# Kernel optimization log

Hardware: AMD Instinct MI355X
Metric: run time of the kernel (lower is better)

## Reference

```python
import jax, jax.numpy as jnp
import numpy as np

D_MODEL = 1024
NUM_HEADS = 16
D_K = D_MODEL // NUM_HEADS


def setup_inputs() -> dict:
    key = jax.random.key(0)
    ks = jax.random.split(key, 9)
    s = 1.0 / np.sqrt(D_MODEL)
    x = jax.random.normal(ks[0], (4, 2048, D_MODEL), dtype=jnp.float32)
    Wq = jax.random.uniform(ks[1], (D_MODEL, D_MODEL), jnp.float32, -s, s)
    bq = jax.random.uniform(ks[2], (D_MODEL,), jnp.float32, -s, s)
    Wk = jax.random.uniform(ks[3], (D_MODEL, D_MODEL), jnp.float32, -s, s)
    bk = jax.random.uniform(ks[4], (D_MODEL,), jnp.float32, -s, s)
    Wv = jax.random.uniform(ks[5], (D_MODEL, D_MODEL), jnp.float32, -s, s)
    bv = jax.random.uniform(ks[6], (D_MODEL,), jnp.float32, -s, s)
    Wo = jax.random.uniform(ks[7], (D_MODEL, D_MODEL), jnp.float32, -s, s)
    bo = jax.random.uniform(ks[8], (D_MODEL,), jnp.float32, -s, s)
    return {"x": x, "Wq": Wq, "bq": bq, "Wk": Wk, "bk": bk,
            "Wv": Wv, "bv": bv, "Wo": Wo, "bo": bo}


def reference(x, Wq, bq, Wk, bk, Wv, bv, Wo, bo):
    B, S, _ = x.shape
    # Linear projections (torch Linear: x @ W.T + b)
    q = x @ Wq.T + bq
    k = x @ Wk.T + bk
    v = x @ Wv.T + bv
    # [B, H, S, d_k]
    q = q.reshape(B, S, NUM_HEADS, D_K).transpose(0, 2, 1, 3)
    k = k.reshape(B, S, NUM_HEADS, D_K).transpose(0, 2, 1, 3)
    v = v.reshape(B, S, NUM_HEADS, D_K).transpose(0, 2, 1, 3)
    score = jnp.einsum('bhqd,bhkd->bhqk', q, k) / jnp.sqrt(jnp.float32(D_K))
    causal = jnp.tril(jnp.ones((S, S), dtype=bool))  # True = keep
    score = jnp.where(causal[None, None], score, -jnp.inf)
    attn = jax.nn.softmax(score, axis=-1)
    out = jnp.einsum('bhqk,bhkd->bhqd', attn, v)
    out = out.transpose(0, 2, 1, 3).reshape(B, S, D_MODEL)
    return out @ Wo.T + bo
```

## Files before the change

### kernel.cpp

```cpp
#include <hip/hip_runtime.h>
#include <hip/hip_bf16.h>
#include <stdint.h>

#define D_MODEL 1024
#define SEQ     2048
#define BATCH   4
#define NHEAD   16
#define DKH     64
#define MTOT    (BATCH * SEQ)

typedef __bf16 bf16x8 __attribute__((ext_vector_type(8)));
typedef __bf16 bf16x4 __attribute__((ext_vector_type(4)));
typedef float  floatx4 __attribute__((ext_vector_type(4)));
typedef short  s16x4  __attribute__((ext_vector_type(4)));

#define GLOAD_LDS16(gp, lp)                                            \
    __builtin_amdgcn_global_load_lds(                                  \
        (const __attribute__((address_space(1))) unsigned int*)(gp),   \
        (__attribute__((address_space(3))) unsigned int*)(lp), 16, 0, 0)

#define MFMA16(a, b, c) __builtin_amdgcn_mfma_f32_16x16x32_bf16(a, b, c, 0, 0, 0)

#if __has_builtin(__builtin_amdgcn_exp2f)
#define EXP2(x) __builtin_amdgcn_exp2f(x)
#else
#define EXP2(x) exp2f(x)
#endif

static __device__ __forceinline__ floatx4 pv_mfma(s16x4 a, s16x4 b, floatx4 c)
{
#if __has_builtin(__builtin_amdgcn_mfma_f32_16x16x16bf16_1k)
    return __builtin_amdgcn_mfma_f32_16x16x16bf16_1k(a, b, c, 0, 0, 0);
#else
    asm("v_mfma_f32_16x16x16_bf16 %0, %1, %2, %0" : "+v"(c) : "v"(a), "v"(b));
    return c;
#endif
}

__global__ __launch_bounds__(256)
void cvt_x_kernel(const float* __restrict__ src, __bf16* __restrict__ dst)
{
    const int i = (blockIdx.x * 256 + threadIdx.x) * 4;
    floatx4 v = *(const floatx4*)(src + i);
    bf16x4 o;
    o[0] = (__bf16)v[0]; o[1] = (__bf16)v[1]; o[2] = (__bf16)v[2]; o[3] = (__bf16)v[3];
    *(bf16x4*)(dst + i) = o;
}

__global__ __launch_bounds__(256)
void cvt_w3_kernel(const float* __restrict__ Wq, const float* __restrict__ Wk,
                   const float* __restrict__ Wv, __bf16* __restrict__ Wcat)
{
    const int z = blockIdx.y;
    const float* src = (z == 0) ? Wq : ((z == 1) ? Wk : Wv);
    const int i = (blockIdx.x * 256 + threadIdx.x) * 4;
    floatx4 v = *(const floatx4*)(src + i);
    bf16x4 o;
    o[0] = (__bf16)v[0]; o[1] = (__bf16)v[1]; o[2] = (__bf16)v[2]; o[3] = (__bf16)v[3];
    *(bf16x4*)(Wcat + (size_t)z * (D_MODEL * D_MODEL) + i) = o;
}

__global__ __launch_bounds__(256)
void qkv_gemm_kernel(const __bf16* __restrict__ xb, const __bf16* __restrict__ Wcat,
                     const float* __restrict__ bq, const float* __restrict__ bk,
                     const float* __restrict__ bv,
                     __bf16* __restrict__ Q, __bf16* __restrict__ K,
                     __bf16* __restrict__ Vt)
{
    __shared__ __align__(16) char smem_raw[128 * 136 * 2];
    __bf16* As = (__bf16*)smem_raw;
    __bf16* Bs = (__bf16*)(smem_raw + 8192);
    __bf16* Cs = (__bf16*)smem_raw;

    const int t    = threadIdx.x;
    const int w    = t >> 6, l = t & 63, quad = l >> 4, r16 = l & 15;
    const int wm   = w & 1, wn = w >> 1;
    const int m0   = blockIdx.y * 128;
    const int n0   = blockIdx.x * 128;
    const int z    = n0 >> 10;
    const float* bias = (z == 0) ? bq : ((z == 1) ? bk : bv);
    __bf16* outQK     = (z == 0) ? Q  : K;
    const float scale = (z == 0) ? 0.18033688011112042f : 1.0f;

    floatx4 acc[4][4];
#pragma unroll
    for (int i = 0; i < 4; ++i)
#pragma unroll
        for (int j = 0; j < 4; ++j) acc[i][j] = (floatx4){0.f, 0.f, 0.f, 0.f};

    const int c0 = t, c1 = t + 256;
    const __bf16* Ag0 = xb   + (size_t)(m0 + (c0 >> 2)) * 1024 + (c0 & 3) * 8;
    const __bf16* Ag1 = xb   + (size_t)(m0 + (c1 >> 2)) * 1024 + (c1 & 3) * 8;
    const __bf16* Bg0 = Wcat + (size_t)(n0 + (c0 >> 2)) * 1024 + (c0 & 3) * 8;
    const __bf16* Bg1 = Wcat + (size_t)(n0 + (c1 >> 2)) * 1024 + (c1 & 3) * 8;
    unsigned int* lAs = (unsigned int*)As;
    unsigned int* lBs = (unsigned int*)Bs;

    for (int k0 = 0; k0 < 1024; k0 += 32) {
        __syncthreads();
        GLOAD_LDS16(Ag0 + k0, lAs + c0 * 4);
        GLOAD_LDS16(Ag1 + k0, lAs + c1 * 4);
        GLOAD_LDS16(Bg0 + k0, lBs + c0 * 4);
        GLOAD_LDS16(Bg1 + k0, lBs + c1 * 4);
        __syncthreads();

        bf16x8 af[4], bfm[4];
#pragma unroll
        for (int i = 0; i < 4; ++i)
            af[i] = *(const bf16x8*)&As[(wm * 64 + i * 16 + r16) * 32 + quad * 8];
#pragma unroll
        for (int j = 0; j < 4; ++j)
            bfm[j] = *(const bf16x8*)&Bs[(wn * 64 + j * 16 + r16) * 32 + quad * 8];
#pragma unroll
        for (int i = 0; i < 4; ++i)
#pragma unroll
            for (int j = 0; j < 4; ++j)
                acc[i][j] = MFMA16(af[i], bfm[j], acc[i][j]);
    }

    __syncthreads();

    if (z == 2) {
#pragma unroll
        for (int i = 0; i < 4; ++i) {
            const int mb = wm * 64 + i * 16 + quad * 4;
#pragma unroll
            for (int j = 0; j < 4; ++j) {
                const int nl = wn * 64 + j * 16 + r16;
                const float bb = bias[(n0 + nl) & 1023];
                bf16x4 p4;
#pragma unroll
                for (int r = 0; r < 4; ++r) p4[r] = (__bf16)(acc[i][j][r] + bb);
                *(bf16x4*)&Cs[nl * 136 + mb] = p4;
            }
        }
    } else {
#pragma unroll
        for (int i = 0; i < 4; ++i) {
            const int mb = wm * 64 + i * 16 + quad * 4;
#pragma unroll
            for (int j = 0; j < 4; ++j) {
                const int nl = wn * 64 + j * 16 + r16;
                const float bb = bias[(n0 + nl) & 1023];
#pragma unroll
                for (int r = 0; r < 4; ++r)
                    Cs[(mb + r) * 136 + nl] =
                        (__bf16)((acc[i][j][r] + bb) * scale);
            }
        }
    }
    __syncthreads();

    const int b  = m0 >> 11;
    if (z == 2) {
#pragma unroll
        for (int k = 0; k < 8; ++k) {
            const int nl = (t >> 4) + k * 16;
            const int ml = (t & 15) * 8;
            bf16x8 row = *(const bf16x8*)&Cs[nl * 136 + ml];
            const int f = (n0 + nl) & 1023, h = f >> 6, d = f & 63;
            const int s = (m0 & 2047) + ml;
            *(bf16x8*)&Vt[((size_t)((b * 16 + h) * 64 + d) << 11) + s] = row;
        }
    } else {
#pragma unroll
        for (int k = 0; k < 8; ++k) {
            const int ml = (t >> 4) + k * 16;
            const int nl = (t & 15) * 8;
            bf16x8 row = *(const bf16x8*)&Cs[ml * 136 + nl];
            const int f = (n0 + nl) & 1023, h = f >> 6, d = f & 63;
            const int s = (m0 & 2047) + ml;
            *(bf16x8*)&outQK[((size_t)(b * 16 + h) << 17) + ((size_t)s << 6) + d]
                = row;
        }
    }
}

__global__ __launch_bounds__(256)
void out_gemm_kernel(const __bf16* __restrict__ A, const __bf16* __restrict__ Wob,
                     const float* __restrict__ bo, float* __restrict__ out)
{
    __shared__ __align__(16) __bf16 As[128 * 32];
    __shared__ __align__(16) __bf16 Bs[128 * 32];

    const int t    = threadIdx.x;
    const int w    = t >> 6, l = t & 63, quad = l >> 4, r16 = l & 15;
    const int wm   = w & 1, wn = w >> 1;
    const int m0   = blockIdx.y * 128;
    const int n0   = blockIdx.x * 128;

    floatx4 acc[4][4];
#pragma unroll
    for (int i = 0; i < 4; ++i)
#pragma unroll
        for (int j = 0; j < 4; ++j) acc[i][j] = (floatx4){0.f, 0.f, 0.f, 0.f};

    const int c0 = t, c1 = t + 256;
    const __bf16* Ag0 = A   + (size_t)(m0 + (c0 >> 2)) * 1024 + (c0 & 3) * 8;
    const __bf16* Ag1 = A   + (size_t)(m0 + (c1 >> 2)) * 1024 + (c1 & 3) * 8;
    const __bf16* Bg0 = Wob + (size_t)(n0 + (c0 >> 2)) * 1024 + (c0 & 3) * 8;
    const __bf16* Bg1 = Wob + (size_t)(n0 + (c1 >> 2)) * 1024 + (c1 & 3) * 8;
    unsigned int* lAs = (unsigned int*)As;
    unsigned int* lBs = (unsigned int*)Bs;

    for (int k0 = 0; k0 < 1024; k0 += 32) {
        __syncthreads();
        GLOAD_LDS16(Ag0 + k0, lAs + c0 * 4);
        GLOAD_LDS16(Ag1 + k0, lAs + c1 * 4);
        GLOAD_LDS16(Bg0 + k0, lBs + c0 * 4);
        GLOAD_LDS16(Bg1 + k0, lBs + c1 * 4);
        __syncthreads();

        bf16x8 af[4], bfm[4];
#pragma unroll
        for (int i = 0; i < 4; ++i)
            af[i] = *(const bf16x8*)&As[(wm * 64 + i * 16 + r16) * 32 + quad * 8];
#pragma unroll
        for (int j = 0; j < 4; ++j)
            bfm[j] = *(const bf16x8*)&Bs[(wn * 64 + j * 16 + r16) * 32 + quad * 8];
#pragma unroll
        for (int i = 0; i < 4; ++i)
#pragma unroll
            for (int j = 0; j < 4; ++j)
                acc[i][j] = MFMA16(af[i], bfm[j], acc[i][j]);
    }

#pragma unroll
    for (int i = 0; i < 4; ++i) {
        const int mg = m0 + wm * 64 + i * 16 + quad * 4;
#pragma unroll
        for (int j = 0; j < 4; ++j) {
            const int ng = n0 + wn * 64 + j * 16 + r16;
            const float bb = bo[ng];
#pragma unroll
            for (int r = 0; r < 4; ++r)
                out[(size_t)(mg + r) * 1024 + ng] = acc[i][j][r] + bb;
        }
    }
}

__global__ __launch_bounds__(256, 4)
void attn_kernel(const __bf16* __restrict__ Qg, const __bf16* __restrict__ Kg,
                 const __bf16* __restrict__ Vtg, __bf16* __restrict__ O)
{
    __shared__ __align__(16) __bf16 Ks[2][64 * 72];
    __shared__ __align__(16) __bf16 Vs[2][64 * 72];

    const int t    = threadIdx.x;
    const int w    = t >> 6, l = t & 63, quad = l >> 4, r16 = l & 15;
    const int bh   = blockIdx.x;
    const int y    = blockIdx.y;
    const int p    = y >> 1, half = y & 1;
    const int qa   = 15 - p, qb = p;
    const size_t base = (size_t)bh * SEQ * DKH;
    const int d0   = 2 * qa + half;
    const int d1   = 2 * qb + half;
    const int nkt  = d0 + 1;
    const int row0 = qa * 128 + half * 64 + w * 16;
    const int row1 = qb * 128 + half * 64 + w * 16;

    const s16x4 ones16 = {(short)0x3F80, (short)0x3F80,
                          (short)0x3F80, (short)0x3F80};

    bf16x8 qf00, qf01, qf10, qf11;
    qf00 = *(const bf16x8*)&Qg[base + (size_t)(row0 + r16) * 64 + quad * 8];
    qf01 = *(const bf16x8*)&Qg[base + (size_t)(row0 + r16) * 64 + 32 + quad * 8];
    qf10 = *(const bf16x8*)&Qg[base + (size_t)(row1 + r16) * 64 + quad * 8];
    qf11 = *(const bf16x8*)&Qg[base + (size_t)(row1 + r16) * 64 + 32 + quad * 8];

    floatx4 o[2][4];
#pragma unroll
    for (int mi = 0; mi < 2; ++mi)
#pragma unroll
        for (int j = 0; j < 4; ++j) o[mi][j] = (floatx4){0.f, 0.f, 0.f, 0.f};
    floatx4 osum[2];
    osum[0] = (floatx4){0.f, 0.f, 0.f, 0.f};
    osum[1] = (floatx4){0.f, 0.f, 0.f, 0.f};

    const int srow = t >> 3;
    const int sg   = (t & 7) * 8;

    bf16x8 kc0, kc1, vc0, vc1;
    kc0 = *(const bf16x8*)&Kg[base + (size_t)srow * 64 + sg];
    kc1 = *(const bf16x8*)&Kg[base + (size_t)(32 + srow) * 64 + sg];
    vc0 = *(const bf16x8*)&Vtg[base + (size_t)srow * 2048 + sg];
    vc1 = *(const bf16x8*)&Vtg[base + (size_t)(32 + srow) * 2048 + sg];

    for (int kt = 0; kt < nkt; ++kt) {
        __bf16* ks = Ks[kt & 1];
        __bf16* vs = Vs[kt & 1];
        *(bf16x8*)&ks[srow * 72 + sg] = kc0;
        *(bf16x8*)&ks[(32 + srow) * 72 + sg] = kc1;
        *(bf16x8*)&vs[srow * 72 + sg] = vc0;
        *(bf16x8*)&vs[(32 + srow) * 72 + sg] = vc1;
        if (kt + 1 < nkt) {
            const int kr = (kt + 1) * 64;
            kc0 = *(const bf16x8*)&Kg[base + (size_t)(kr + srow) * 64 + sg];
            kc1 = *(const bf16x8*)&Kg[base + (size_t)(kr + 32 + srow) * 64 + sg];
            vc0 = *(const bf16x8*)&Vtg[base + (size_t)srow * 2048 + kr + sg];
            vc1 = *(const bf16x8*)&Vtg[base + (size_t)(32 + srow) * 2048 + kr + sg];
        }
        __syncthreads();

        const bool a1 = (kt <= d1);
        __builtin_amdgcn_s_setprio(1);
        bf16x8 kf0, kf1;
#pragma unroll
        for (int j = 0; j < 4; ++j) {
            kf0 = *(const bf16x8*)&ks[(j * 16 + r16) * 72 + quad * 8];
            kf1 = *(const bf16x8*)&ks[(j * 16 + r16) * 72 + 32 + quad * 8];
            floatx4 z0 = (floatx4){0.f, 0.f, 0.f, 0.f};
            floatx4 z1 = (floatx4){0.f, 0.f, 0.f, 0.f};
            z0 = MFMA16(kf0, qf00, z0);
            z0 = MFMA16(kf1, qf01, z0);
            if (a1) {
                z1 = MFMA16(kf0, qf10, z1);
                z1 = MFMA16(kf1, qf11, z1);
            }
            const int kg = kt * 64 + j * 16 + quad * 4;
            bf16x4 pb0, pb1;
            if (kt < d0) {
#pragma unroll
                for (int r = 0; r < 4; ++r)
                    pb0[r] = (__bf16)EXP2(z0[r]);
            } else {
                const int qg0 = row0 + r16;
#pragma unroll
                for (int r = 0; r < 4; ++r) {
                    float pp = 0.f;
                    if (kg + r <= qg0) pp = EXP2(z0[r]);
                    pb0[r] = (__bf16)pp;
                }
            }
            s16x4 pa0 = __builtin_bit_cast(s16x4, pb0);
            s16x4 pa1;
            if (a1) {
                if (kt < d1) {
#pragma unroll
                    for (int r = 0; r < 4; ++r)
                        pb1[r] = (__bf16)EXP2(z1[r]);
                } else {
                    const int qg1 = row1 + r16;
#pragma unroll
                    for (int r = 0; r < 4; ++r) {
                        float pp = 0.f;
                        if (kg + r <= qg1) pp = EXP2(z1[r]);
                        pb1[r] = (__bf16)pp;
                    }
                }
                pa1 = __builtin_bit_cast(s16x4, pb1);
            }
            osum[0] = pv_mfma(pa0, ones16, osum[0]);
            if (a1) osum[1] = pv_mfma(pa1, ones16, osum[1]);
#pragma unroll
            for (int jd = 0; jd < 4; ++jd) {
                const s16x4 vv =
                    *(const s16x4*)&vs[(jd * 16 + r16) * 72 + j * 16 + quad * 4];
                o[0][jd] = pv_mfma(pa0, vv, o[0][jd]);
                if (a1) o[1][jd] = pv_mfma(pa1, vv, o[1][jd]);
            }
        }
        __builtin_amdgcn_s_setprio(0);
    }

    const int b = bh >> 4, h = bh & 15;
#pragma unroll
    for (int mi = 0; mi < 2; ++mi) {
        const int rowb = (mi == 0) ? row0 : row1;
#pragma unroll
        for (int r = 0; r < 4; ++r) {
            const int qrow = rowb + quad * 4 + r;
            const float inv = 1.f / osum[mi][r];
#pragma unroll
            for (int jd = 0; jd < 4; ++jd) {
                const int d = jd * 16 + r16;
                O[((size_t)(b * SEQ + qrow) * D_MODEL) + h * 64 + d] =
                    (__bf16)(o[mi][jd][r] * inv);
            }
        }
    }
}

extern "C" void kernel_launch(void* const* d_in, const int* in_sizes, int n_in,
                              void* d_out, int out_size, void* d_ws, size_t ws_size,
                              hipStream_t stream)
{
    (void)in_sizes; (void)n_in; (void)out_size; (void)ws_size;
    const float* x  = (const float*)d_in[0];
    const float* Wq = (const float*)d_in[1];
    const float* bq = (const float*)d_in[2];
    const float* Wk = (const float*)d_in[3];
    const float* bk = (const float*)d_in[4];
    const float* Wv = (const float*)d_in[5];
    const float* bv = (const float*)d_in[6];
    const float* Wo = (const float*)d_in[7];
    const float* bo = (const float*)d_in[8];
    float* out = (float*)d_out;

    const size_t n_elem = (size_t)MTOT * D_MODEL;
    const int    w_n    = D_MODEL * D_MODEL;
    __bf16* Qb  = (__bf16*)d_out;
    __bf16* xb  = Qb + n_elem;
    __bf16* Kb   = (__bf16*)d_ws;
    __bf16* Vtb  = Kb + n_elem;
    __bf16* Ab   = Vtb + n_elem;
    __bf16* Wcat = Ab;
    __bf16* Wob  = Kb;

    cvt_x_kernel<<<MTOT * D_MODEL / 1024, 256, 0, stream>>>(x, xb);
    cvt_w3_kernel<<<dim3(w_n / 1024, 3), 256, 0, stream>>>(Wq, Wk, Wv, Wcat);
    qkv_gemm_kernel<<<dim3(24, 64), 256, 0, stream>>>(xb, Wcat, bq, bk, bv,
                                                      Qb, Kb, Vtb);
    attn_kernel<<<dim3(64, 16), 256, 0, stream>>>(Qb, Kb, Vtb, Ab);
    cvt_x_kernel<<<w_n / 1024, 256, 0, stream>>>(Wo, Wob);
    out_gemm_kernel<<<dim3(8, 64), 256, 0, stream>>>(Ab, Wob, bo, out);
}
```

Baseline: 253.0 us.

## Double-buffer GEMM LDS tiles with XOR swizzle and merge conversion kernels

```diff
diff --git a/kernel.cpp b/kernel.cpp
--- a/kernel.cpp
+++ b/kernel.cpp
@@ -38,6 +38,30 @@
 }
 
 __global__ __launch_bounds__(256)
+void cvt_pre_kernel(const float* __restrict__ x, const float* __restrict__ Wq,
+                    const float* __restrict__ Wk, const float* __restrict__ Wv,
+                    __bf16* __restrict__ xb, __bf16* __restrict__ Wcat)
+{
+    int bid = blockIdx.x;
+    const float* src;
+    __bf16* dst;
+    if (bid < 8192) {
+        src = x;  dst = xb;
+    } else {
+        bid -= 8192;
+        const int z = bid >> 10;
+        bid &= 1023;
+        src = (z == 0) ? Wq : ((z == 1) ? Wk : Wv);
+        dst = Wcat + (size_t)z * (D_MODEL * D_MODEL);
+    }
+    const int i = (bid * 256 + threadIdx.x) * 4;
+    floatx4 v = *(const floatx4*)(src + i);
+    bf16x4 o;
+    o[0] = (__bf16)v[0]; o[1] = (__bf16)v[1]; o[2] = (__bf16)v[2]; o[3] = (__bf16)v[3];
+    *(bf16x4*)(dst + i) = o;
+}
+
+__global__ __launch_bounds__(256)
 void cvt_x_kernel(const float* __restrict__ src, __bf16* __restrict__ dst)
 {
     const int i = (blockIdx.x * 256 + threadIdx.x) * 4;
@@ -47,18 +71,29 @@
     *(bf16x4*)(dst + i) = o;
 }
 
-__global__ __launch_bounds__(256)
-void cvt_w3_kernel(const float* __restrict__ Wq, const float* __restrict__ Wk,
-                   const float* __restrict__ Wv, __bf16* __restrict__ Wcat)
-{
-    const int z = blockIdx.y;
-    const float* src = (z == 0) ? Wq : ((z == 1) ? Wk : Wv);
-    const int i = (blockIdx.x * 256 + threadIdx.x) * 4;
-    floatx4 v = *(const floatx4*)(src + i);
-    bf16x4 o;
-    o[0] = (__bf16)v[0]; o[1] = (__bf16)v[1]; o[2] = (__bf16)v[2]; o[3] = (__bf16)v[3];
-    *(bf16x4*)(Wcat + (size_t)z * (D_MODEL * D_MODEL) + i) = o;
-}
+#define G_STAGE(SMEM, BUFOFF, KOFF)                                           \
+    GLOAD_LDS16(Ag0 + (KOFF), (unsigned int*)((SMEM) + (BUFOFF)) + c0 * 4);   \
+    GLOAD_LDS16(Ag1 + (KOFF), (unsigned int*)((SMEM) + (BUFOFF)) + c1 * 4);   \
+    GLOAD_LDS16(Bg0 + (KOFF), (unsigned int*)((SMEM) + (BUFOFF) + 8192) + c0 * 4); \
+    GLOAD_LDS16(Bg1 + (KOFF), (unsigned int*)((SMEM) + (BUFOFF) + 8192) + c1 * 4);
+
+#define G_COMPUTE(SMEM, BUFOFF)                                               \
+    {                                                                         \
+        const __bf16* As_ = (const __bf16*)((SMEM) + (BUFOFF));               \
+        const __bf16* Bs_ = (const __bf16*)((SMEM) + (BUFOFF) + 8192);        \
+        bf16x8 af[4], bfm[4];                                                 \
+        _Pragma("unroll")                                                     \
+        for (int i = 0; i < 4; ++i)                                           \
+            af[i] = *(const bf16x8*)&As_[(wm * 64 + i * 16 + r16) * 32 + fsw];\
+        _Pragma("unroll")                                                     \
+        for (int j = 0; j < 4; ++j)                                           \
+            bfm[j] = *(const bf16x8*)&Bs_[(wn * 64 + j * 16 + r16) * 32 + fsw];\
+        _Pragma("unroll")                                                     \
+        for (int i = 0; i < 4; ++i)                                           \
+            _Pragma("unroll")                                                 \
+            for (int j = 0; j < 4; ++j)                                       \
+                acc[i][j] = MFMA16(af[i], bfm[j], acc[i][j]);                 \
+    }
 
 __global__ __launch_bounds__(256)
 void qkv_gemm_kernel(const __bf16* __restrict__ xb, const __bf16* __restrict__ Wcat,
@@ -68,8 +103,6 @@
                      __bf16* __restrict__ Vt)
 {
     __shared__ __align__(16) char smem_raw[128 * 136 * 2];
-    __bf16* As = (__bf16*)smem_raw;
-    __bf16* Bs = (__bf16*)(smem_raw + 8192);
     __bf16* Cs = (__bf16*)smem_raw;
 
     const int t    = threadIdx.x;
@@ -89,36 +122,26 @@
         for (int j = 0; j < 4; ++j) acc[i][j] = (floatx4){0.f, 0.f, 0.f, 0.f};
 
     const int c0 = t, c1 = t + 256;
-    const __bf16* Ag0 = xb   + (size_t)(m0 + (c0 >> 2)) * 1024 + (c0 & 3) * 8;
-    const __bf16* Ag1 = xb   + (size_t)(m0 + (c1 >> 2)) * 1024 + (c1 & 3) * 8;
-    const __bf16* Bg0 = Wcat + (size_t)(n0 + (c0 >> 2)) * 1024 + (c0 & 3) * 8;
-    const __bf16* Bg1 = Wcat + (size_t)(n0 + (c1 >> 2)) * 1024 + (c1 & 3) * 8;
-    unsigned int* lAs = (unsigned int*)As;
-    unsigned int* lBs = (unsigned int*)Bs;
-
-    for (int k0 = 0; k0 < 1024; k0 += 32) {
+    const int row0 = c0 >> 2, s0 = (((c0 & 3) ^ (row0 & 3))) * 8;
+    const int row1 = c1 >> 2, s1 = (((c1 & 3) ^ (row1 & 3))) * 8;
+    const __bf16* Ag0 = xb   + (size_t)(m0 + row0) * 1024 + s0;
+    const __bf16* Ag1 = xb   + (size_t)(m0 + row1) * 1024 + s1;
+    const __bf16* Bg0 = Wcat + (size_t)(n0 + row0) * 1024 + s0;
+    const __bf16* Bg1 = Wcat + (size_t)(n0 + row1) * 1024 + s1;
+
+    const int fsw = (quad ^ (r16 & 3)) * 8;
+
+    G_STAGE(smem_raw, 0, 0);
+    __syncthreads();
+
+    for (int k0 = 0; k0 < 1024; k0 += 64) {
+        if (k0 + 32 < 1024) { G_STAGE(smem_raw, 16384, k0 + 32); }
+        G_COMPUTE(smem_raw, 0);
         __syncthreads();
-        GLOAD_LDS16(Ag0 + k0, lAs + c0 * 4);
-        GLOAD_LDS16(Ag1 + k0, lAs + c1 * 4);
-        GLOAD_LDS16(Bg0 + k0, lBs + c0 * 4);
-        GLOAD_LDS16(Bg1 + k0, lBs + c1 * 4);
+        if (k0 + 64 < 1024) { G_STAGE(smem_raw, 0, k0 + 64); }
+        G_COMPUTE(smem_raw, 16384);
         __syncthreads();
-
-        bf16x8 af[4], bfm[4];
-#pragma unroll
-        for (int i = 0; i < 4; ++i)
-            af[i] = *(const bf16x8*)&As[(wm * 64 + i * 16 + r16) * 32 + quad * 8];
-#pragma unroll
-        for (int j = 0; j < 4; ++j)
-            bfm[j] = *(const bf16x8*)&Bs[(wn * 64 + j * 16 + r16) * 32 + quad * 8];
-#pragma unroll
-        for (int i = 0; i < 4; ++i)
-#pragma unroll
-            for (int j = 0; j < 4; ++j)
-                acc[i][j] = MFMA16(af[i], bfm[j], acc[i][j]);
-    }
-
-    __syncthreads();
+    }
 
     if (z == 2) {
 #pragma unroll
@@ -180,8 +203,7 @@
 void out_gemm_kernel(const __bf16* __restrict__ A, const __bf16* __restrict__ Wob,
                      const float* __restrict__ bo, float* __restrict__ out)
 {
-    __shared__ __align__(16) __bf16 As[128 * 32];
-    __shared__ __align__(16) __bf16 Bs[128 * 32];
+    __shared__ __align__(16) char smem_raw[4 * 8192];
 
     const int t    = threadIdx.x;
     const int w    = t >> 6, l = t & 63, quad = l >> 4, r16 = l & 15;
@@ -196,33 +218,24 @@
         for (int j = 0; j < 4; ++j) acc[i][j] = (floatx4){0.f, 0.f, 0.f, 0.f};
 
     const int c0 = t, c1 = t + 256;
-    const __bf16* Ag0 = A   + (size_t)(m0 + (c0 >> 2)) * 1024 + (c0 & 3) * 8;
-    const __bf16* Ag1 = A   + (size_t)(m0 + (c1 >> 2)) * 1024 + (c1 & 3) * 8;
-    const __bf16* Bg0 = Wob + (size_t)(n0 + (c0 >> 2)) * 1024 + (c0 & 3) * 8;
-    const __bf16* Bg1 = Wob + (size_t)(n0 + (c1 >> 2)) * 1024 + (c1 & 3) * 8;
-    unsigned int* lAs = (unsigned int*)As;
-    unsigned int* lBs = (unsigned int*)Bs;
-
-    for (int k0 = 0; k0 < 1024; k0 += 32) {
+    const int row0 = c0 >> 2, s0 = (((c0 & 3) ^ (row0 & 3))) * 8;
+    const int row1 = c1 >> 2, s1 = (((c1 & 3) ^ (row1 & 3))) * 8;
+    const __bf16* Ag0 = A   + (size_t)(m0 + row0) * 1024 + s0;
+    const __bf16* Ag1 = A   + (size_t)(m0 + row1) * 1024 + s1;
+    const __bf16* Bg0 = Wob + (size_t)(n0 + row0) * 1024 + s0;
+    const __bf16* Bg1 = Wob + (size_t)(n0 + row1) * 1024 + s1;
+    const int fsw = (quad ^ (r16 & 3)) * 8;
+
+    G_STAGE(smem_raw, 0, 0);
+    __syncthreads();
+
+    for (int k0 = 0; k0 < 1024; k0 += 64) {
+        if (k0 + 32 < 1024) { G_STAGE(smem_raw, 16384, k0 + 32); }
+        G_COMPUTE(smem_raw, 0);
         __syncthreads();
-        GLOAD_LDS16(Ag0 + k0, lAs + c0 * 4);
-        GLOAD_LDS16(Ag1 + k0, lAs + c1 * 4);
-        GLOAD_LDS16(Bg0 + k0, lBs + c0 * 4);
-        GLOAD_LDS16(Bg1 + k0, lBs + c1 * 4);
+        if (k0 + 64 < 1024) { G_STAGE(smem_raw, 0, k0 + 64); }
+        G_COMPUTE(smem_raw, 16384);
         __syncthreads();
-
-        bf16x8 af[4], bfm[4];
-#pragma unroll
-        for (int i = 0; i < 4; ++i)
-            af[i] = *(const bf16x8*)&As[(wm * 64 + i * 16 + r16) * 32 + quad * 8];
-#pragma unroll
-        for (int j = 0; j < 4; ++j)
-            bfm[j] = *(const bf16x8*)&Bs[(wn * 64 + j * 16 + r16) * 32 + quad * 8];
-#pragma unroll
-        for (int i = 0; i < 4; ++i)
-#pragma unroll
-            for (int j = 0; j < 4; ++j)
-                acc[i][j] = MFMA16(af[i], bfm[j], acc[i][j]);
     }
 
 #pragma unroll
@@ -407,8 +420,7 @@
     __bf16* Wcat = Ab;
     __bf16* Wob  = Kb;
 
-    cvt_x_kernel<<<MTOT * D_MODEL / 1024, 256, 0, stream>>>(x, xb);
-    cvt_w3_kernel<<<dim3(w_n / 1024, 3), 256, 0, stream>>>(Wq, Wk, Wv, Wcat);
+    cvt_pre_kernel<<<8192 + 3072, 256, 0, stream>>>(x, Wq, Wk, Wv, xb, Wcat);
     qkv_gemm_kernel<<<dim3(24, 64), 256, 0, stream>>>(xb, Wcat, bq, bk, bv,
                                                       Qb, Kb, Vtb);
     attn_kernel<<<dim3(64, 16), 256, 0, stream>>>(Qb, Kb, Vtb, Ab);
```

After: 256.6 us. Within noise of the previous version (+1.4%).
